# Kernel optimization log

Hardware: AMD Instinct MI355X
Metric: run time of the kernel (lower is better)

The kernel has to match this reference:

```python
import jax, jax.numpy as jnp
import numpy as np

N = 100000
E = 3200000
IN_C, HID_C, LAT_C = 256, 256, 64
NEG_SLOPE = 0.01  # torch nn.LeakyReLU default


def gcn_conv(x, W, b, src, dst, norm):
    # x: [N, Fin], W: [Fin, Fout], src/dst: [E'] (self-loops included), norm: [E']
    h = x @ W                                   # [N, Fout]
    msg = h[src] * norm[:, None]                # gather + scale
    out = jax.ops.segment_sum(msg, dst, num_segments=N)  # scatter-add
    return out + b


def _with_self_loops(edge_index):
    loop = jnp.arange(N, dtype=edge_index.dtype)
    src = jnp.concatenate([edge_index[0], loop])
    dst = jnp.concatenate([edge_index[1], loop])
    return src, dst


def _sym_norm(src, dst):
    ones = jnp.ones(src.shape[0], dtype=jnp.float32)
    deg = jax.ops.segment_sum(ones, dst, num_segments=N)  # in-degree incl. self-loop
    dis = jnp.where(deg > 0, jax.lax.rsqrt(deg), 0.0)
    return dis[src] * dis[dst]


def setup_inputs() -> dict:
    key = jax.random.key(0)
    ks = jax.random.split(key, 8)
    x = jax.random.normal(ks[0], (N, IN_C), dtype=jnp.float32)
    edge_index = jax.random.randint(ks[1], (2, E), 0, N, dtype=jnp.int64)
    s = 1.0 / np.sqrt(IN_C)
    W_shared = jax.random.uniform(ks[2], (IN_C, HID_C), jnp.float32, -s, s)
    b_shared = jnp.zeros((HID_C,), jnp.float32)
    s2 = 1.0 / np.sqrt(HID_C)
    W_mu = jax.random.uniform(ks[3], (HID_C, LAT_C), jnp.float32, -s2, s2)
    b_mu = jnp.zeros((LAT_C,), jnp.float32)
    W_lv = jax.random.uniform(ks[4], (HID_C, LAT_C), jnp.float32, -s2, s2)
    b_lv = jnp.zeros((LAT_C,), jnp.float32)
    return {"x": x, "edge_index": edge_index,
            "W_shared": W_shared, "b_shared": b_shared,
            "W_mu": W_mu, "b_mu": b_mu,
            "W_lv": W_lv, "b_lv": b_lv}


def reference(x, W_shared, b_shared, W_mu, b_mu, W_lv, b_lv, edge_index):
    src, dst = _with_self_loops(edge_index)
    norm = _sym_norm(src, dst)
    h = gcn_conv(x, W_shared, b_shared, src, dst, norm)
    h = jnp.where(h >= 0, h, NEG_SLOPE * h)     # LeakyReLU(0.01)
    mu = gcn_conv(h, W_mu, b_mu, src, dst, norm)
    logvar = jnp.minimum(gcn_conv(h, W_lv, b_lv, src, dst, norm), 10.0)
    return (mu, logvar)
```

## Files before the change

### kernel.cpp

```cpp
#include <hip/hip_runtime.h>
#include <hip/hip_bf16.h>

#define N_NODES 100000
#define FEAT 256
#define NEG_SLOPE 0.01f
#define NBUK 782
#define BCAP 5120
#define NBB 256
#define NGB 782

using bf16x8 = __attribute__((ext_vector_type(8))) __bf16;
using f32x4  = __attribute__((ext_vector_type(4))) float;
using ushort8 = __attribute__((ext_vector_type(8))) unsigned short;

__device__ __forceinline__ unsigned short f2bf(float f) {
    unsigned int u = __float_as_uint(f);
    unsigned int r = u + 0x7fffu + ((u >> 16) & 1u);
    return (unsigned short)(r >> 16);
}
__device__ __forceinline__ void gload_lds16(const void* g, void* l) {
    __builtin_amdgcn_global_load_lds(
        (const __attribute__((address_space(1))) void*)g,
        (__attribute__((address_space(3))) void*)l, 16, 0, 0);
}
__device__ __forceinline__ void accum_row(float* acc, uint4 u, float qv) {
    unsigned int dw[4] = {u.x, u.y, u.z, u.w};
#pragma unroll
    for (int d = 0; d < 4; ++d) {
        float f0, f1, f2, f3;
        asm("v_cvt_f32_ubyte0 %0, %1" : "=v"(f0) : "v"(dw[d]));
        asm("v_cvt_f32_ubyte1 %0, %1" : "=v"(f1) : "v"(dw[d]));
        asm("v_cvt_f32_ubyte2 %0, %1" : "=v"(f2) : "v"(dw[d]));
        asm("v_cvt_f32_ubyte3 %0, %1" : "=v"(f3) : "v"(dw[d]));
        acc[d * 4 + 0] += qv * f0;
        acc[d * 4 + 1] += qv * f1;
        acc[d * 4 + 2] += qv * f2;
        acc[d * 4 + 3] += qv * f3;
    }
}

__global__ void k_init(const int* __restrict__ ei, int* __restrict__ flag,
                       int* __restrict__ bcnt, float* __restrict__ qd,
                       float* __restrict__ qsB,
                       const float* __restrict__ Wsh, const float* __restrict__ Wmu,
                       const float* __restrict__ Wlv,
                       unsigned short* __restrict__ Wt, unsigned short* __restrict__ Wct) {
    const int b = blockIdx.x, t = threadIdx.x;
    if (b == 0) {
        if (t == 0) {
            int nz = 0;
            for (int i = 0; i < 64; ++i) nz |= ei[2 * i + 1];
            *flag = (nz == 0) ? 2 : 1;
            qd[N_NODES]  = 0.f;
            qsB[N_NODES] = 0.f;
        }
        for (int i = t; i < NBUK; i += 256) bcnt[i] = 0;
    } else {
        const int i = (b - 1) * 256 + t;
        {
            const int n = i >> 8, k = i & 255;
            Wt[(size_t)n * 256 + k] = f2bf(Wsh[(size_t)k * 256 + n]);
        }
        if (i < 128 * 256) {
            const int n = i >> 8, k = i & 255;
            const float v = (n < 64) ? Wmu[(size_t)k * 64 + n] : Wlv[(size_t)k * 64 + (n - 64)];
            Wct[(size_t)n * 256 + k] = f2bf(v);
        }
    }
}

__global__ void __launch_bounds__(512) k_phaseA(
        const int* __restrict__ ei, const int* __restrict__ flag,
        int* __restrict__ bcnt, int2* __restrict__ ebuf, int E,
        const float* __restrict__ A, const unsigned short* __restrict__ Bt,
        unsigned char* __restrict__ q8, float* __restrict__ qs, int M) {
    __shared__ int lcnt[NBUK];
    __shared__ int lbase[NBUK];
    __shared__ __align__(16) unsigned short lA[128 * 32];
    __shared__ __align__(16) unsigned short lB[256 * 32];
    __shared__ float rmax[128][4];
    const int t = threadIdx.x;

    if (blockIdx.x < NBB) {
        const int s = *flag;
        for (int i = t; i < NBUK; i += 512) lcnt[i] = 0;
        __syncthreads();
        const int per = (E + NBB - 1) / NBB;
        const int e0 = blockIdx.x * per;
        const int e1 = min(e0 + per, E);
        for (int e = e0 + t; e < e1; e += 512) {
            const int d = ei[(size_t)(E + e) * s];
            atomicAdd(&lcnt[d >> 7], 1);
        }
        __syncthreads();
        for (int i = t; i < NBUK; i += 512) {
            const int c = lcnt[i];
            lbase[i] = c ? atomicAdd(&bcnt[i], c) : 0;
            lcnt[i] = 0;
        }
        __syncthreads();
        for (int e = e0 + t; e < e1; e += 512) {
            const int sv = ei[(size_t)e * s];
            const int dv = ei[(size_t)(E + e) * s];
            const int b = dv >> 7;
            const int p = lbase[b] + atomicAdd(&lcnt[b], 1);
            if (p < BCAP) ebuf[(size_t)b * BCAP + p] = make_int2(sv, dv);
        }
        return;
    }

    const int bid = blockIdx.x - NBB;
    const int w = t >> 6, l = t & 63;
    const int wr = w >> 2, wc = w & 3;
    const int l15 = l & 15, lh = l >> 4;
    const int rowbase = bid * 128;

    f32x4 acc[4][4];
#pragma unroll
    for (int mi = 0; mi < 4; ++mi)
#pragma unroll
        for (int nj = 0; nj < 4; ++nj)
            acc[mi][nj] = (f32x4){0.f, 0.f, 0.f, 0.f};

    const int ar = t >> 2, sl = t & 3;
    int grA = rowbase + ar; if (grA > M - 1) grA = M - 1;
    const float* aptr = A + (size_t)grA * FEAT + sl * 8;

#pragma unroll 1
    for (int ks = 0; ks < 8; ++ks) {
        const int k0 = ks * 32;
        gload_lds16(Bt + ((size_t)ar * FEAT + k0 + sl * 8), &lB[(size_t)t * 8]);
        gload_lds16(Bt + ((size_t)(128 + ar) * FEAT + k0 + sl * 8), &lB[(size_t)(512 + t) * 8]);
        float4 f0 = *reinterpret_cast<const float4*>(aptr + k0);
        float4 f1 = *reinterpret_cast<const float4*>(aptr + k0 + 4);
        ushort8 ua;
        ua[0] = f2bf(f0.x); ua[1] = f2bf(f0.y); ua[2] = f2bf(f0.z); ua[3] = f2bf(f0.w);
        ua[4] = f2bf(f1.x); ua[5] = f2bf(f1.y); ua[6] = f2bf(f1.z); ua[7] = f2bf(f1.w);
        *reinterpret_cast<ushort8*>(&lA[(size_t)ar * 32 + sl * 8]) = ua;
        asm volatile("s_waitcnt vmcnt(0)" ::: "memory");
        __syncthreads();

        bf16x8 a[4];
#pragma unroll
        for (int mi = 0; mi < 4; ++mi)
            a[mi] = *reinterpret_cast<const bf16x8*>(&lA[(wr * 64 + mi * 16 + l15) * 32 + lh * 8]);
#pragma unroll
        for (int nj = 0; nj < 4; ++nj) {
            bf16x8 b = *reinterpret_cast<const bf16x8*>(&lB[(wc * 64 + nj * 16 + l15) * 32 + lh * 8]);
#pragma unroll
            for (int mi = 0; mi < 4; ++mi)
                acc[mi][nj] = __builtin_amdgcn_mfma_f32_16x16x32_bf16(a[mi], b, acc[mi][nj], 0, 0, 0);
        }
        __syncthreads();
    }

#pragma unroll
    for (int mi = 0; mi < 4; ++mi) {
#pragma unroll
        for (int r = 0; r < 4; ++r) {
            const int rl = wr * 64 + mi * 16 + lh * 4 + r;
            float m = 0.f;
#pragma unroll
            for (int nj = 0; nj < 4; ++nj) m = fmaxf(m, fabsf(acc[mi][nj][r]));
            m = fmaxf(m, __shfl_xor(m, 1, 64));
            m = fmaxf(m, __shfl_xor(m, 2, 64));
            m = fmaxf(m, __shfl_xor(m, 4, 64));
            m = fmaxf(m, __shfl_xor(m, 8, 64));
            if (l15 == 0) rmax[rl][wc] = m;
        }
    }
    __syncthreads();
#pragma unroll
    for (int mi = 0; mi < 4; ++mi) {
#pragma unroll
        for (int r = 0; r < 4; ++r) {
            const int rl = wr * 64 + mi * 16 + lh * 4 + r;
            const int row = rowbase + rl;
            const float fm = fmaxf(fmaxf(rmax[rl][0], rmax[rl][1]),
                                   fmaxf(rmax[rl][2], rmax[rl][3]));
            const float inv = (fm > 0.f) ? (127.0f / fm) : 0.f;
            if (row < M) {
                if (wc == 0 && l15 == 0) qs[row] = fm * (1.0f / 127.0f);
#pragma unroll
                for (int nj = 0; nj < 4; ++nj) {
                    int qv = (int)rintf(acc[mi][nj][r] * inv) + 128;
                    qv = min(max(qv, 0), 255);
                    q8[(size_t)row * 256 + wc * 64 + nj * 16 + l15] = (unsigned char)qv;
                }
            }
        }
    }
}

__global__ void k_csr(const int2* __restrict__ ebuf, const int* __restrict__ bcnt,
                      int* __restrict__ csr, int* __restrict__ rowp0,
                      int* __restrict__ rowe, float* __restrict__ dis,
                      const float* __restrict__ qsA, float* __restrict__ qd) {
    __shared__ int ncnt[128];
    __shared__ int nexcl[128];
    __shared__ int nstart[128];
    const int t = threadIdx.x;
    const int b = blockIdx.x;
    const int nb = b << 7;
    if (t < 128) ncnt[t] = 0;
    __syncthreads();
    const int cnt = min(bcnt[b], BCAP);
    const int2* eb = ebuf + (size_t)b * BCAP;
    for (int i = t; i < cnt; i += 256) atomicAdd(&ncnt[eb[i].y - nb], 1);
    __syncthreads();
    const int own = (t < 128) ? ncnt[t] : 0;
    const int region = (t < 128) ? ((own + 4) & ~3) : 0;
    if (t < 128) nexcl[t] = region;
    __syncthreads();
    for (int off = 1; off < 128; off <<= 1) {
        int v = 0;
        if (t < 128 && t >= off) v = nexcl[t - off];
        __syncthreads();
        if (t < 128) nexcl[t] += v;
        __syncthreads();
    }
    if (t < 128) {
        const int excl = nexcl[t] - region;
        const int v = nb + t;
        if (v < N_NODES) {
            rowp0[v] = b * BCAP + excl;
            rowe[v]  = b * BCAP + excl + region;
            const float dv = rsqrtf((float)(own + 1));
            dis[v] = dv;
            qd[v]  = qsA[v] * dv;
            if (excl < BCAP) csr[(size_t)b * BCAP + excl] = v;
            for (int i = own + 1; i < region; ++i)
                if (excl + i < BCAP) csr[(size_t)b * BCAP + excl + i] = N_NODES;
        }
        nstart[t] = excl + 1;
        ncnt[t] = 0;
    }
    __syncthreads();
    for (int i = t; i < cnt; i += 256) {
        const int2 e = eb[i];
        const int li = e.y - nb;
        const int p = nstart[li] + atomicAdd(&ncnt[li], 1);
        if (p < BCAP) csr[(size_t)b * BCAP + p] = e.x;
    }
}

__global__ void k_gemm128q(const unsigned short* __restrict__ A,
                           const unsigned short* __restrict__ Bt,
                           unsigned char* __restrict__ q8, float* __restrict__ qs,
                           const float* __restrict__ scale, int M) {
    __shared__ __align__(16) unsigned short lA[64 * 32];
    __shared__ __align__(16) unsigned short lB[128 * 32];
    __shared__ float rmax[64][4];
    const int t = threadIdx.x;
    const int w = t >> 6, l = t & 63;
    const int l15 = l & 15, lh = l >> 4;
    const int rowbase = blockIdx.x * 64;

    f32x4 acc[4][2];
#pragma unroll
    for (int mi = 0; mi < 4; ++mi)
#pragma unroll
        for (int nj = 0; nj < 2; ++nj)
            acc[mi][nj] = (f32x4){0.f, 0.f, 0.f, 0.f};

    const int sr = t >> 2, sl = t & 3;
    int grA = rowbase + sr; if (grA > M - 1) grA = M - 1;

#pragma unroll 1
    for (int ks = 0; ks < 8; ++ks) {
        const int k0 = ks * 32;
        gload_lds16(A + ((size_t)grA * FEAT + k0 + sl * 8), &lA[(size_t)t * 8]);
#pragma unroll
        for (int j = 0; j < 2; ++j)
            gload_lds16(Bt + ((size_t)(j * 64 + sr) * FEAT + k0 + sl * 8),
                        &lB[(size_t)j * 2048 + (size_t)t * 8]);
        asm volatile("s_waitcnt vmcnt(0)" ::: "memory");
        __syncthreads();

        bf16x8 a[4];
#pragma unroll
        for (int mi = 0; mi < 4; ++mi)
            a[mi] = *reinterpret_cast<const bf16x8*>(&lA[(mi * 16 + l15) * 32 + lh * 8]);
#pragma unroll
        for (int nj = 0; nj < 2; ++nj) {
            bf16x8 b = *reinterpret_cast<const bf16x8*>(&lB[(w * 32 + nj * 16 + l15) * 32 + lh * 8]);
#pragma unroll
            for (int mi = 0; mi < 4; ++mi)
                acc[mi][nj] = __builtin_amdgcn_mfma_f32_16x16x32_bf16(a[mi], b, acc[mi][nj], 0, 0, 0);
        }
        __syncthreads();
    }

#pragma unroll
    for (int mi = 0; mi < 4; ++mi) {
#pragma unroll
        for (int r = 0; r < 4; ++r) {
            const int rl = mi * 16 + lh * 4 + r;
            int row = rowbase + rl; if (row > M - 1) row = M - 1;
            const float sc = scale[row];
            float m = 0.f;
#pragma unroll
            for (int nj = 0; nj < 2; ++nj) {
                acc[mi][nj][r] *= sc;
                m = fmaxf(m, fabsf(acc[mi][nj][r]));
            }
            m = fmaxf(m, __shfl_xor(m, 1, 64));
            m = fmaxf(m, __shfl_xor(m, 2, 64));
            m = fmaxf(m, __shfl_xor(m, 4, 64));
            m = fmaxf(m, __shfl_xor(m, 8, 64));
            if (l15 == 0) rmax[rl][w] = m;
        }
    }
    __syncthreads();
#pragma unroll
    for (int mi = 0; mi < 4; ++mi) {
#pragma unroll
        for (int r = 0; r < 4; ++r) {
            const int rl = mi * 16 + lh * 4 + r;
            const int row = rowbase + rl;
            const float fm = fmaxf(fmaxf(rmax[rl][0], rmax[rl][1]),
                                   fmaxf(rmax[rl][2], rmax[rl][3]));
            const float inv = (fm > 0.f) ? (127.0f / fm) : 0.f;
            if (row < M) {
                if (w == 0 && l15 == 0) qs[row] = fm * (1.0f / 127.0f);
#pragma unroll
                for (int nj = 0; nj < 2; ++nj) {
                    int qv = (int)rintf(acc[mi][nj][r] * inv) + 128;
                    qv = min(max(qv, 0), 255);
                    q8[(size_t)row * 128 + w * 32 + nj * 16 + l15] = (unsigned char)qv;
                }
            }
        }
    }
}

__global__ void k_agg1(const unsigned char* __restrict__ q8, const float* __restrict__ qd,
                       const int* __restrict__ rowp0, const int* __restrict__ rowe,
                       const int* __restrict__ csr,
                       const float* __restrict__ dis, const float* __restrict__ bias,
                       unsigned short* __restrict__ hout) {
    const int w = threadIdx.x >> 6, l = threadIdx.x & 63;
    const int v = blockIdx.x * 4 + w;
    if (v >= N_NODES) return;
    const int q = l >> 4, li = l & 15;
    const int p0 = rowp0[v], p1 = rowe[v];

    float acc[16];
#pragma unroll
    for (int j = 0; j < 16; ++j) acc[j] = 0.f;
    float sqs = 0.f;

    for (int g = p0 + q * 4; g < p1; g += 16) {
        const int4 s4 = *reinterpret_cast<const int4*>(&csr[g]);
        const float q0 = qd[s4.x], q1 = qd[s4.y], q2 = qd[s4.z], q3 = qd[s4.w];
        uint4 u0 = *reinterpret_cast<const uint4*>(&q8[(size_t)s4.x * 256 + li * 16]);
        uint4 u1 = *reinterpret_cast<const uint4*>(&q8[(size_t)s4.y * 256 + li * 16]);
        uint4 u2 = *reinterpret_cast<const uint4*>(&q8[(size_t)s4.z * 256 + li * 16]);
        uint4 u3 = *reinterpret_cast<const uint4*>(&q8[(size_t)s4.w * 256 + li * 16]);
        sqs += q0 + q1 + q2 + q3;
        accum_row(acc, u0, q0);
        accum_row(acc, u1, q1);
        accum_row(acc, u2, q2);
        accum_row(acc, u3, q3);
    }
#pragma unroll
    for (int j = 0; j < 16; ++j) acc[j] -= 128.f * sqs;

#pragma unroll
    for (int j = 0; j < 16; ++j) acc[j] += __shfl_xor(acc[j], 16, 64);
#pragma unroll
    for (int j = 0; j < 16; ++j) acc[j] += __shfl_xor(acc[j], 32, 64);

    if (l < 16) {
        const float dv = dis[v];
        const int c = l * 16;
        ushort8 r0, r1;
#pragma unroll
        for (int j = 0; j < 8; ++j) {
            float o = dv * acc[j] + bias[c + j];
            o = (o >= 0.f) ? o : NEG_SLOPE * o;
            r0[j] = f2bf(o);
        }
#pragma unroll
        for (int j = 0; j < 8; ++j) {
            float o = dv * acc[8 + j] + bias[c + 8 + j];
            o = (o >= 0.f) ? o : NEG_SLOPE * o;
            r1[j] = f2bf(o);
        }
        *reinterpret_cast<ushort8*>(&hout[(size_t)v * FEAT + c])     = r0;
        *reinterpret_cast<ushort8*>(&hout[(size_t)v * FEAT + c + 8]) = r1;
    }
}

__global__ void k_agg2(const unsigned char* __restrict__ q8, const float* __restrict__ qs,
                       const int* __restrict__ rowp0, const int* __restrict__ rowe,
                       const int* __restrict__ csr,
                       const float* __restrict__ dis,
                       const float* __restrict__ bmu, const float* __restrict__ blv,
                       float* __restrict__ out) {
    const int w = threadIdx.x >> 6, l = threadIdx.x & 63;
    const int v = blockIdx.x * 4 + w;
    if (v >= N_NODES) return;
    const int e = l >> 3, li = l & 7;
    const int p0 = rowp0[v], p1 = rowe[v];

    float acc[16];
#pragma unroll
    for (int j = 0; j < 16; ++j) acc[j] = 0.f;
    float sqs = 0.f;

    for (int g = p0 + e * 4; g < p1; g += 32) {
        const int4 s4 = *reinterpret_cast<const int4*>(&csr[g]);
        const float q0 = qs[s4.x], q1 = qs[s4.y], q2 = qs[s4.z], q3 = qs[s4.w];
        uint4 u0 = *reinterpret_cast<const uint4*>(&q8[(size_t)s4.x * 128 + li * 16]);
        uint4 u1 = *reinterpret_cast<const uint4*>(&q8[(size_t)s4.y * 128 + li * 16]);
        uint4 u2 = *reinterpret_cast<const uint4*>(&q8[(size_t)s4.z * 128 + li * 16]);
        uint4 u3 = *reinterpret_cast<const uint4*>(&q8[(size_t)s4.w * 128 + li * 16]);
        sqs += q0 + q1 + q2 + q3;
        accum_row(acc, u0, q0);
        accum_row(acc, u1, q1);
        accum_row(acc, u2, q2);
        accum_row(acc, u3, q3);
    }
#pragma unroll
    for (int j = 0; j < 16; ++j) acc[j] -= 128.f * sqs;

#pragma unroll
    for (int j = 0; j < 16; ++j) acc[j] += __shfl_xor(acc[j], 8, 64);
#pragma unroll
    for (int j = 0; j < 16; ++j) acc[j] += __shfl_xor(acc[j], 16, 64);
#pragma unroll
    for (int j = 0; j < 16; ++j) acc[j] += __shfl_xor(acc[j], 32, 64);

    if (l < 8) {
        const float dv = dis[v];
        const int c = l * 16;
        float o[16];
        if (c < 64) {
#pragma unroll
            for (int j = 0; j < 16; ++j) o[j] = dv * acc[j] + bmu[c + j];
            float* dst = &out[(size_t)v * 64 + c];
#pragma unroll
            for (int k = 0; k < 4; ++k) {
                float4 f = {o[k * 4], o[k * 4 + 1], o[k * 4 + 2], o[k * 4 + 3]};
                *reinterpret_cast<float4*>(dst + k * 4) = f;
            }
        } else {
            const int cc = c - 64;
#pragma unroll
            for (int j = 0; j < 16; ++j) o[j] = fminf(dv * acc[j] + blv[cc + j], 10.0f);
            float* dst = &out[(size_t)N_NODES * 64 + (size_t)v * 64 + cc];
#pragma unroll
            for (int k = 0; k < 4; ++k) {
                float4 f = {o[k * 4], o[k * 4 + 1], o[k * 4 + 2], o[k * 4 + 3]};
                *reinterpret_cast<float4*>(dst + k * 4) = f;
            }
        }
    }
}

extern "C" void kernel_launch(void* const* d_in, const int* in_sizes, int n_in,
                              void* d_out, int out_size, void* d_ws, size_t ws_size,
                              hipStream_t stream) {
    const float* x   = (const float*)d_in[0];
    const int*   ei  = (const int*)d_in[1];
    const float* Wsh = (const float*)d_in[2];
    const float* bsh = (const float*)d_in[3];
    const float* Wmu = (const float*)d_in[4];
    const float* bmu = (const float*)d_in[5];
    const float* Wlv = (const float*)d_in[6];
    const float* blv = (const float*)d_in[7];
    const int E = in_sizes[1] / 2;

    char* base = (char*)d_ws;
    size_t off = 0;
    auto take = [&](size_t bytes) -> char* {
        char* r = base + off;
        off += (bytes + 511) & ~(size_t)511;
        return r;
    };
    int*   flag  = (int*)take(4);
    int*   bcnt  = (int*)take((size_t)NBUK * 4);
    int*   rowp0 = (int*)take((size_t)N_NODES * 4);
    int*   rowe  = (int*)take((size_t)N_NODES * 4);
    float* dis   = (float*)take((size_t)N_NODES * 4);
    float* qd    = (float*)take(((size_t)N_NODES + 1) * 4);
    int*   csr   = (int*)take((size_t)NBUK * BCAP * 4);
    unsigned short* bufA = (unsigned short*)take((size_t)N_NODES * FEAT * 2);
    unsigned short* Wt   = (unsigned short*)take(256 * 256 * 2);
    unsigned short* Wct  = (unsigned short*)take(128 * 256 * 2);
    unsigned char* q8A = (unsigned char*)take(((size_t)N_NODES + 1) * 256);
    float*         qsA = (float*)take(((size_t)N_NODES + 1) * 4);
    unsigned char* q8B = (unsigned char*)take(((size_t)N_NODES + 1) * 128);
    float*         qsB = (float*)take(((size_t)N_NODES + 1) * 4);
    int2* ebuf = (int2*)bufA;

    k_init<<<257, 256, 0, stream>>>(ei, flag, bcnt, qd, qsB, Wsh, Wmu, Wlv, Wt, Wct);
    k_phaseA<<<NBB + NGB, 512, 0, stream>>>(ei, flag, bcnt, ebuf, E, x, Wt, q8A, qsA, N_NODES);
    k_csr<<<NBUK, 256, 0, stream>>>(ebuf, bcnt, csr, rowp0, rowe, dis, qsA, qd);
    k_agg1<<<(N_NODES + 3) / 4, 256, 0, stream>>>(q8A, qd, rowp0, rowe, csr, dis, bsh, bufA);
    k_gemm128q<<<(N_NODES + 63) / 64, 256, 0, stream>>>(bufA, Wct, q8B, qsB, dis, N_NODES);
    k_agg2<<<(N_NODES + 3) / 4, 256, 0, stream>>>(q8B, qsB, rowp0, rowe, csr, dis, bmu, blv, (float*)d_out);
}
```

Measured before the change: 379.7 us.

## Sort edges in LDS before bucket scatter and use raw buffer loads in aggregation

The edge-bucketing blocks now handle a fixed chunk of edges and run a local prefix sum over bucket counts. They sort the edges into shared memory, then write them to the global bucket buffer in contiguous runs instead of scattered writes. The smem arrays are merged into one union buffer so LDS use stays bounded, and the block count now scales with E. Both aggregation kernels replace pointer gathers with inline-asm buffer_load instructions using 32-bit offsets, issuing all eight loads before a single explicit vmcnt(0) wait. This may reduce address arithmetic, but it removes the compiler's freedom to schedule and overlap those loads.

```diff
diff --git a/kernel.cpp b/kernel.cpp
--- a/kernel.cpp
+++ b/kernel.cpp
@@ -6,12 +6,13 @@
 #define NEG_SLOPE 0.01f
 #define NBUK 782
 #define BCAP 5120
-#define NBB 256
+#define PERB 3125
 #define NGB 782
 
 using bf16x8 = __attribute__((ext_vector_type(8))) __bf16;
 using f32x4  = __attribute__((ext_vector_type(4))) float;
 using ushort8 = __attribute__((ext_vector_type(8))) unsigned short;
+using u32x4  = __attribute__((ext_vector_type(4))) unsigned int;
 
 __device__ __forceinline__ unsigned short f2bf(float f) {
     unsigned int u = __float_as_uint(f);
@@ -23,7 +24,16 @@
         (const __attribute__((address_space(1))) void*)g,
         (__attribute__((address_space(3))) void*)l, 16, 0, 0);
 }
-__device__ __forceinline__ void accum_row(float* acc, uint4 u, float qv) {
+__device__ __forceinline__ u32x4 make_srsrc(const void* p, unsigned bytes) {
+    unsigned long long a = (unsigned long long)p;
+    u32x4 r;
+    r.x = (unsigned)a;
+    r.y = (unsigned)(a >> 32);
+    r.z = bytes;
+    r.w = 0x00020000u;
+    return r;
+}
+__device__ __forceinline__ void accum_row(float* acc, u32x4 u, float qv) {
     unsigned int dw[4] = {u.x, u.y, u.z, u.w};
 #pragma unroll
     for (int d = 0; d < 4; ++d) {
@@ -71,30 +81,38 @@
 
 __global__ void __launch_bounds__(512) k_phaseA(
         const int* __restrict__ ei, const int* __restrict__ flag,
-        int* __restrict__ bcnt, int2* __restrict__ ebuf, int E,
+        int* __restrict__ bcnt, int2* __restrict__ ebuf, int E, int nbb,
         const float* __restrict__ A, const unsigned short* __restrict__ Bt,
         unsigned char* __restrict__ q8, float* __restrict__ qs, int M) {
-    __shared__ int lcnt[NBUK];
-    __shared__ int lbase[NBUK];
-    __shared__ __align__(16) unsigned short lA[128 * 32];
-    __shared__ __align__(16) unsigned short lB[256 * 32];
-    __shared__ float rmax[128][4];
+    __shared__ __align__(16) unsigned char smem[36480];
     const int t = threadIdx.x;
 
-    if (blockIdx.x < NBB) {
+    if (blockIdx.x < nbb) {
+        int2* sorted = (int2*)smem;
+        int*  lcnt   = (int*)(smem + 25088);
+        int*  lofs   = (int*)(smem + 29184);
+        int*  lbase  = (int*)(smem + 33280);
         const int s = *flag;
-        for (int i = t; i < NBUK; i += 512) lcnt[i] = 0;
-        __syncthreads();
-        const int per = (E + NBB - 1) / NBB;
-        const int e0 = blockIdx.x * per;
-        const int e1 = min(e0 + per, E);
-        for (int e = e0 + t; e < e1; e += 512) {
-            const int d = ei[(size_t)(E + e) * s];
-            atomicAdd(&lcnt[d >> 7], 1);
-        }
-        __syncthreads();
+        const int e0 = blockIdx.x * PERB;
+        const int e1 = min(e0 + PERB, E);
+        const int cnt = e1 - e0;
+        for (int i = t; i < 1024; i += 512) lcnt[i] = 0;
+        __syncthreads();
+        for (int e = e0 + t; e < e1; e += 512)
+            atomicAdd(&lcnt[ei[(size_t)(E + e) * s] >> 7], 1);
+        __syncthreads();
+        lofs[t] = lcnt[t]; lofs[t + 512] = lcnt[t + 512];
+        __syncthreads();
+        for (int off = 1; off < 1024; off <<= 1) {
+            const int a  = (t >= off) ? lofs[t - off] : 0;
+            const int b2 = (t + 512 >= off) ? lofs[t + 512 - off] : 0;
+            __syncthreads();
+            lofs[t] += a; lofs[t + 512] += b2;
+            __syncthreads();
+        }
         for (int i = t; i < NBUK; i += 512) {
             const int c = lcnt[i];
+            lofs[i] -= c;
             lbase[i] = c ? atomicAdd(&bcnt[i], c) : 0;
             lcnt[i] = 0;
         }
@@ -103,13 +121,23 @@
             const int sv = ei[(size_t)e * s];
             const int dv = ei[(size_t)(E + e) * s];
             const int b = dv >> 7;
-            const int p = lbase[b] + atomicAdd(&lcnt[b], 1);
-            if (p < BCAP) ebuf[(size_t)b * BCAP + p] = make_int2(sv, dv);
+            const int p = lofs[b] + atomicAdd(&lcnt[b], 1);
+            sorted[p] = make_int2(sv, dv);
+        }
+        __syncthreads();
+        for (int j = t; j < cnt; j += 512) {
+            const int2 e = sorted[j];
+            const int b = e.y >> 7;
+            const int p = lbase[b] + (j - lofs[b]);
+            if (p < BCAP) ebuf[(size_t)b * BCAP + p] = e;
         }
         return;
     }
 
-    const int bid = blockIdx.x - NBB;
+    unsigned short* lA = (unsigned short*)smem;
+    unsigned short* lB = (unsigned short*)(smem + 8192);
+    float (*rmax)[4]   = reinterpret_cast<float(*)[4]>(smem + 24576);
+    const int bid = blockIdx.x - nbb;
     const int w = t >> 6, l = t & 63;
     const int wr = w >> 2, wc = w & 3;
     const int l15 = l & 15, lh = l >> 4;
@@ -344,6 +372,9 @@
     if (v >= N_NODES) return;
     const int q = l >> 4, li = l & 15;
     const int p0 = rowp0[v], p1 = rowe[v];
+    const u32x4 rs_row = make_srsrc(q8, (unsigned)(N_NODES + 1) * 256u);
+    const u32x4 rs_qd  = make_srsrc(qd, (unsigned)(N_NODES + 1) * 4u);
+    const unsigned li16 = (unsigned)li * 16u;
 
     float acc[16];
 #pragma unroll
@@ -352,11 +383,27 @@
 
     for (int g = p0 + q * 4; g < p1; g += 16) {
         const int4 s4 = *reinterpret_cast<const int4*>(&csr[g]);
-        const float q0 = qd[s4.x], q1 = qd[s4.y], q2 = qd[s4.z], q3 = qd[s4.w];
-        uint4 u0 = *reinterpret_cast<const uint4*>(&q8[(size_t)s4.x * 256 + li * 16]);
-        uint4 u1 = *reinterpret_cast<const uint4*>(&q8[(size_t)s4.y * 256 + li * 16]);
-        uint4 u2 = *reinterpret_cast<const uint4*>(&q8[(size_t)s4.z * 256 + li * 16]);
-        uint4 u3 = *reinterpret_cast<const uint4*>(&q8[(size_t)s4.w * 256 + li * 16]);
+        u32x4 u0, u1, u2, u3;
+        float q0, q1, q2, q3;
+        asm volatile("buffer_load_dwordx4 %0, %1, %2, 0 offen"
+                     : "=v"(u0) : "v"(((unsigned)s4.x << 8) + li16), "s"(rs_row));
+        asm volatile("buffer_load_dwordx4 %0, %1, %2, 0 offen"
+                     : "=v"(u1) : "v"(((unsigned)s4.y << 8) + li16), "s"(rs_row));
+        asm volatile("buffer_load_dwordx4 %0, %1, %2, 0 offen"
+                     : "=v"(u2) : "v"(((unsigned)s4.z << 8) + li16), "s"(rs_row));
+        asm volatile("buffer_load_dwordx4 %0, %1, %2, 0 offen"
+                     : "=v"(u3) : "v"(((unsigned)s4.w << 8) + li16), "s"(rs_row));
+        asm volatile("buffer_load_dword %0, %1, %2, 0 offen"
+                     : "=v"(q0) : "v"((unsigned)s4.x << 2), "s"(rs_qd));
+        asm volatile("buffer_load_dword %0, %1, %2, 0 offen"
+                     : "=v"(q1) : "v"((unsigned)s4.y << 2), "s"(rs_qd));
+        asm volatile("buffer_load_dword %0, %1, %2, 0 offen"
+                     : "=v"(q2) : "v"((unsigned)s4.z << 2), "s"(rs_qd));
+        asm volatile("buffer_load_dword %0, %1, %2, 0 offen"
+                     : "=v"(q3) : "v"((unsigned)s4.w << 2), "s"(rs_qd));
+        asm volatile("s_waitcnt vmcnt(0)"
+                     : "+v"(u0), "+v"(u1), "+v"(u2), "+v"(u3),
+                       "+v"(q0), "+v"(q1), "+v"(q2), "+v"(q3));
         sqs += q0 + q1 + q2 + q3;
         accum_row(acc, u0, q0);
         accum_row(acc, u1, q1);
@@ -403,6 +450,9 @@
     if (v >= N_NODES) return;
     const int e = l >> 3, li = l & 7;
     const int p0 = rowp0[v], p1 = rowe[v];
+    const u32x4 rs_row = make_srsrc(q8, (unsigned)(N_NODES + 1) * 128u);
+    const u32x4 rs_qs  = make_srsrc(qs, (unsigned)(N_NODES + 1) * 4u);
+    const unsigned li16 = (unsigned)li * 16u;
 
     float acc[16];
 #pragma unroll
@@ -411,11 +461,27 @@
 
     for (int g = p0 + e * 4; g < p1; g += 32) {
         const int4 s4 = *reinterpret_cast<const int4*>(&csr[g]);
-        const float q0 = qs[s4.x], q1 = qs[s4.y], q2 = qs[s4.z], q3 = qs[s4.w];
-        uint4 u0 = *reinterpret_cast<const uint4*>(&q8[(size_t)s4.x * 128 + li * 16]);
-        uint4 u1 = *reinterpret_cast<const uint4*>(&q8[(size_t)s4.y * 128 + li * 16]);
-        uint4 u2 = *reinterpret_cast<const uint4*>(&q8[(size_t)s4.z * 128 + li * 16]);
-        uint4 u3 = *reinterpret_cast<const uint4*>(&q8[(size_t)s4.w * 128 + li * 16]);
+        u32x4 u0, u1, u2, u3;
+        float q0, q1, q2, q3;
+        asm volatile("buffer_load_dwordx4 %0, %1, %2, 0 offen"
+                     : "=v"(u0) : "v"(((unsigned)s4.x << 7) + li16), "s"(rs_row));
+        asm volatile("buffer_load_dwordx4 %0, %1, %2, 0 offen"
+                     : "=v"(u1) : "v"(((unsigned)s4.y << 7) + li16), "s"(rs_row));
+        asm volatile("buffer_load_dwordx4 %0, %1, %2, 0 offen"
+                     : "=v"(u2) : "v"(((unsigned)s4.z << 7) + li16), "s"(rs_row));
+        asm volatile("buffer_load_dwordx4 %0, %1, %2, 0 offen"
+                     : "=v"(u3) : "v"(((unsigned)s4.w << 7) + li16), "s"(rs_row));
+        asm volatile("buffer_load_dword %0, %1, %2, 0 offen"
+                     : "=v"(q0) : "v"((unsigned)s4.x << 2), "s"(rs_qs));
+        asm volatile("buffer_load_dword %0, %1, %2, 0 offen"
+                     : "=v"(q1) : "v"((unsigned)s4.y << 2), "s"(rs_qs));
+        asm volatile("buffer_load_dword %0, %1, %2, 0 offen"
+                     : "=v"(q2) : "v"((unsigned)s4.z << 2), "s"(rs_qs));
+        asm volatile("buffer_load_dword %0, %1, %2, 0 offen"
+                     : "=v"(q3) : "v"((unsigned)s4.w << 2), "s"(rs_qs));
+        asm volatile("s_waitcnt vmcnt(0)"
+                     : "+v"(u0), "+v"(u1), "+v"(u2), "+v"(u3),
+                       "+v"(q0), "+v"(q1), "+v"(q2), "+v"(q3));
         sqs += q0 + q1 + q2 + q3;
         accum_row(acc, u0, q0);
         accum_row(acc, u1, q1);
@@ -471,6 +537,7 @@
     const float* Wlv = (const float*)d_in[6];
     const float* blv = (const float*)d_in[7];
     const int E = in_sizes[1] / 2;
+    const int nbb = (E + PERB - 1) / PERB;
 
     char* base = (char*)d_ws;
     size_t off = 0;
@@ -496,7 +563,7 @@
     int2* ebuf = (int2*)bufA;
 
     k_init<<<257, 256, 0, stream>>>(ei, flag, bcnt, qd, qsB, Wsh, Wmu, Wlv, Wt, Wct);
-    k_phaseA<<<NBB + NGB, 512, 0, stream>>>(ei, flag, bcnt, ebuf, E, x, Wt, q8A, qsA, N_NODES);
+    k_phaseA<<<nbb + NGB, 512, 0, stream>>>(ei, flag, bcnt, ebuf, E, nbb, x, Wt, q8A, qsA, N_NODES);
     k_csr<<<NBUK, 256, 0, stream>>>(ebuf, bcnt, csr, rowp0, rowe, dis, qsA, qd);
     k_agg1<<<(N_NODES + 3) / 4, 256, 0, stream>>>(q8A, qd, rowp0, rowe, csr, dis, bsh, bufA);
     k_gemm128q<<<(N_NODES + 63) / 64, 256, 0, stream>>>(bufA, Wct, q8B, qsB, dis, N_NODES);
```

New measurement: 369.3 us. 1.03x faster.
